# Kernel optimization log

Hardware: AMD Instinct MI355X
Metric: run time of the kernel (lower is better)

The kernel has to match this reference:

```python
import jax, jax.numpy as jnp
import numpy as np

HEAD_DIM = 128
INFTY_APPROX = 1e+30
ROTARY_BASE = 10000.0

B, T, M = 2, 2048, 1024
H = M // HEAD_DIM  # 8


def setup_inputs() -> dict:
    key = jax.random.key(0)
    ks = jax.random.split(key, 5)
    x = jax.random.normal(ks[0], (B, T, M), dtype=jnp.float32)
    # mu-param inits: wq zeros in the original; use small random here for a
    # non-degenerate numerical baseline, scaled like kv_init = d_model**-0.5
    scale = M ** (-0.5)
    wq = jax.random.normal(ks[1], (M, H, HEAD_DIM), dtype=jnp.float32) * scale
    wk = jax.random.normal(ks[2], (M, H, HEAD_DIM), dtype=jnp.float32) * scale
    wv = jax.random.normal(ks[3], (M, H, HEAD_DIM), dtype=jnp.float32) * scale
    wo = jax.random.normal(ks[4], (H, HEAD_DIM, M), dtype=jnp.float32) * scale
    return {"x": x, "wq": wq, "wk": wk, "wv": wv, "wo": wo}


def _rotary(x, base=ROTARY_BASE):
    # x: [..., T, W]; non-interpretable RoPE over even/odd halves of W
    length, width = x.shape[-2], x.shape[-1]
    half = width // 2
    positions = jnp.arange(length)[:, None].astype(x.dtype)          # [T,1]
    ang_freqs = jnp.power(base, -jnp.arange(half) / half)[None, :]   # [1,half]
    radians = positions * ang_freqs                                  # [T,half]
    cos = jnp.cos(radians).astype(x.dtype)
    sin = jnp.sin(radians).astype(x.dtype)
    even, odd = jnp.split(x, 2, axis=-1)
    return jnp.concatenate([even * cos - odd * sin,
                            even * sin + odd * cos], axis=-1)


def _fractional_rotary(x):
    # rotary on first half of head dim, passthrough on the rest
    rot, skip = jnp.split(x, 2, axis=-1)
    return jnp.concatenate([_rotary(rot), skip], axis=-1)


def reference(x, wq, wk, wv, wo):
    q = jnp.einsum('bim,mhd->bhid', x, wq)
    k = jnp.einsum('bim,mhd->bhid', x, wk)
    v = jnp.einsum('bim,mhd->bhid', x, wv)
    q = _fractional_rotary(q)
    k = _fractional_rotary(k)
    # mu-param attention: scale by 1/HEAD_DIM (not 1/sqrt(D))
    s = jnp.einsum('bhid,bhjd->bhij', q, k) / HEAD_DIM
    i = jnp.arange(T)[:, None]
    j = jnp.arange(T)[None, :]
    mask = (i < j).astype(s.dtype)  # strictly-upper-triangular
    s = s - jnp.asarray(INFTY_APPROX, dtype=s.dtype) * mask
    p = jax.nn.softmax(s, axis=-1)
    o = jnp.einsum('bhij,bhjd->bhid', p, v)
    r = jnp.einsum('bhid,hdm->bim', o, wo)
    return r
```

## Files before the change

kernel.cpp:

```cpp
#include <hip/hip_runtime.h>

#define T_SEQ 2048
#define MDL   1024
#define NH    8
#define HD    128

typedef __bf16 bf16;
typedef __bf16 bf16x8 __attribute__((ext_vector_type(8)));
typedef __bf16 bf16x4 __attribute__((ext_vector_type(4)));
typedef float  f32x4  __attribute__((ext_vector_type(4)));

#define GLB(p) ((const __attribute__((address_space(1))) void*)(p))
#define LDS(p) ((__attribute__((address_space(3))) void*)(p))


__global__ __launch_bounds__(256) void convert_x_kernel(
    const float* __restrict__ x, bf16* __restrict__ xb)
{
    size_t i = ((size_t)blockIdx.x * 256 + threadIdx.x) * 8;
    float4 v0 = *(const float4*)(x + i);
    float4 v1 = *(const float4*)(x + i + 4);
    bf16x8 o;
    o[0]=(bf16)v0.x; o[1]=(bf16)v0.y; o[2]=(bf16)v0.z; o[3]=(bf16)v0.w;
    o[4]=(bf16)v1.x; o[5]=(bf16)v1.y; o[6]=(bf16)v1.z; o[7]=(bf16)v1.w;
    *(bf16x8*)(xb + i) = o;
}

__global__ __launch_bounds__(256) void transpose_w_kernel(
    const float* __restrict__ wq, const float* __restrict__ wk,
    const float* __restrict__ wv, const float* __restrict__ wo,
    bf16* __restrict__ Wt, bf16* __restrict__ Wot)
{
    __shared__ bf16 t_lds[64 * 72];
    const int bx = blockIdx.x;
    const int sec = bx >> 8;
    const int tile = bx & 255;
    const int k0 = (tile >> 4) * 64, n0 = (tile & 15) * 64;
    const float* src = sec == 0 ? wq : sec == 1 ? wk : sec == 2 ? wv : wo;
    bf16* dst = sec < 3 ? (Wt + (size_t)sec * MDL * MDL) : Wot;

    const int tid = threadIdx.x;
    const int ir = tid >> 2, jc = (tid & 3) * 16;
    const float* sp = src + (size_t)(k0 + ir) * MDL + n0 + jc;
    #pragma unroll
    for (int c = 0; c < 4; ++c) {
        float4 v = *(const float4*)(sp + c * 4);
        bf16x4 o; o[0]=(bf16)v.x; o[1]=(bf16)v.y; o[2]=(bf16)v.z; o[3]=(bf16)v.w;
        *(bf16x4*)&t_lds[ir * 72 + jc + c * 4] = o;
    }
    __syncthreads();
    bf16x8 o0, o1;
    #pragma unroll
    for (int jj = 0; jj < 8; ++jj) {
        o0[jj] = t_lds[(jc + jj) * 72 + ir];
        o1[jj] = t_lds[(jc + 8 + jj) * 72 + ir];
    }
    bf16* dp = dst + (size_t)(n0 + ir) * MDL + k0 + jc;
    *(bf16x8*)dp = o0;
    *(bf16x8*)(dp + 8) = o1;
}

__global__ __launch_bounds__(256) void qkv_rope_kernel(
    const bf16* __restrict__ xb, const bf16* __restrict__ Wt,
    bf16* __restrict__ Qb, bf16* __restrict__ Kt, bf16* __restrict__ Vt)
{
    __shared__ bf16 smem[8192];
    bf16* a_lds = smem;
    bf16* b_lds = smem + 4096;

    const int tid = threadIdx.x, bx = blockIdx.x;
    const int nt = bx % 24, mt = bx / 24;
    const int n0 = nt * 128, m0 = mt * 128;
    const int section = n0 >> 10;
    const int h = (n0 & 1023) >> 7;

    const int lane = tid & 63, w = tid >> 6;
    const int quad = lane >> 4, l15 = lane & 15;
    const int wr = w >> 1, wc = w & 1;
    const int lrow = lane >> 2, lsub = lane & 3;

    const bf16* gA = xb + (size_t)m0 * MDL + lsub * 8;
    const bf16* gB = Wt + (size_t)n0 * MDL + lsub * 8;

    f32x4 acc[4][4] = {};

    for (int k0 = 0; k0 < MDL; k0 += 32) {
        #pragma unroll
        for (int i = 0; i < 2; ++i) {
            const int ch = w * 2 + i;
            const int row = ch * 16 + lrow;
            __builtin_amdgcn_global_load_lds(GLB(gA + (size_t)row * MDL + k0),
                                             LDS(&a_lds[ch * 16 * 32]), 16, 0, 0);
            __builtin_amdgcn_global_load_lds(GLB(gB + (size_t)row * MDL + k0),
                                             LDS(&b_lds[ch * 16 * 32]), 16, 0, 0);
        }
        __syncthreads();

        bf16x8 af[4], bfr[4];
        #pragma unroll
        for (int mi = 0; mi < 4; ++mi)
            af[mi] = *(const bf16x8*)&a_lds[(wr * 64 + mi * 16 + l15) * 32 + quad * 8];
        #pragma unroll
        for (int ni = 0; ni < 4; ++ni)
            bfr[ni] = *(const bf16x8*)&b_lds[(wc * 64 + ni * 16 + l15) * 32 + quad * 8];
        #pragma unroll
        for (int mi = 0; mi < 4; ++mi)
            #pragma unroll
            for (int ni = 0; ni < 4; ++ni)
                acc[mi][ni] = __builtin_amdgcn_mfma_f32_16x16x32_bf16(af[mi], bfr[ni], acc[mi][ni], 0, 0, 0);
        __syncthreads();
    }

    const int bdx = m0 >> 11;
    const int t0 = m0 & (T_SEQ - 1);
    const int bh = bdx * NH + h;

    if (section == 2) {
        #pragma unroll
        for (int c = 0; c < 2; ++c) {
            if (wc == c) {
                #pragma unroll
                for (int mi = 0; mi < 4; ++mi)
                    #pragma unroll
                    for (int r = 0; r < 4; ++r) {
                        int t_loc = wr * 64 + mi * 16 + quad * 4 + r;
                        int base = (t_loc >> 3) * 512 + (t_loc & 7);
                        #pragma unroll
                        for (int ni = 0; ni < 4; ++ni)
                            smem[base + (ni * 16 + l15) * 8] = (bf16)acc[mi][ni][r];
                    }
            }
            __syncthreads();
            {
                const int t8 = tid >> 4;
                bf16* vp = Vt + ((size_t)(bh * 32 + (t0 >> 6) + (t8 >> 3))) * 8192
                              + (t8 & 7) * 1024 + c * 512 + (tid & 15) * 32;
                #pragma unroll
                for (int k = 0; k < 4; ++k)
                    *(bf16x8*)(vp + k * 8) = *(const bf16x8*)&smem[tid * 32 + k * 8];
            }
            __syncthreads();
        }
        return;
    }

    float fr_n[2];
    #pragma unroll
    for (int ni = 0; ni < 2; ++ni)
        fr_n[ni] = __expf(-(float)(ni * 16 + l15) * 0.28782313662425573f);

    if (section == 0) {
        #pragma unroll
        for (int mi = 0; mi < 4; ++mi) {
            #pragma unroll
            for (int r = 0; r < 4; ++r) {
                int t = t0 + wr * 64 + mi * 16 + quad * 4 + r;
                bf16* orow = Qb + ((size_t)bh * T_SEQ + t) * HD;
                if (wc == 0) {
                    #pragma unroll
                    for (int ni = 0; ni < 2; ++ni) {
                        int d = ni * 16 + l15;
                        float ang = (float)t * fr_n[ni];
                        float sn = __sinf(ang), cs = __cosf(ang);
                        float ev = acc[mi][ni][r];
                        float ov = acc[mi][ni + 2][r];
                        orow[d]      = (bf16)(ev * cs - ov * sn);
                        orow[d + 32] = (bf16)(ev * sn + ov * cs);
                    }
                } else {
                    #pragma unroll
                    for (int ni = 0; ni < 4; ++ni)
                        orow[64 + ni * 16 + l15] = (bf16)acc[mi][ni][r];
                }
            }
        }
    } else {
        #pragma unroll
        for (int c = 0; c < 2; ++c) {
            if (wr == c) {
                #pragma unroll
                for (int mi = 0; mi < 4; ++mi) {
                    #pragma unroll
                    for (int r = 0; r < 4; ++r) {
                        int tl = mi * 16 + quad * 4 + r;
                        int t = t0 + c * 64 + tl;
                        if (wc == 0) {
                            #pragma unroll
                            for (int ni = 0; ni < 2; ++ni) {
                                int d = ni * 16 + l15;
                                float ang = (float)t * fr_n[ni];
                                float sn = __sinf(ang), cs = __cosf(ang);
                                float ev = acc[mi][ni][r];
                                float ov = acc[mi][ni + 2][r];
                                smem[(d >> 3) * 512 + tl * 8 + (d & 7)] = (bf16)(ev * cs - ov * sn);
                                int d2 = d + 32;
                                smem[(d2 >> 3) * 512 + tl * 8 + (d2 & 7)] = (bf16)(ev * sn + ov * cs);
                            }
                        } else {
                            #pragma unroll
                            for (int ni = 0; ni < 4; ++ni) {
                                int d = 64 + ni * 16 + l15;
                                smem[(d >> 3) * 512 + tl * 8 + (d & 7)] = (bf16)acc[mi][ni][r];
                            }
                        }
                    }
                }
            }
            __syncthreads();
            {
                bf16* kp = Kt + ((size_t)(bh * 32 + (t0 >> 6) + c)) * 8192 + tid * 32;
                #pragma unroll
                for (int k = 0; k < 4; ++k)
                    *(bf16x8*)(kp + k * 8) = *(const bf16x8*)&smem[tid * 32 + k * 8];
            }
            __syncthreads();
        }
    }
}

__global__ __launch_bounds__(256) void attn_kernel(
    const bf16* __restrict__ Qb, const bf16* __restrict__ Kt,
    const bf16* __restrict__ Vt, bf16* __restrict__ PO, float* __restrict__ Pl)
{
    __shared__ bf16 k_lds[8192];
    __shared__ bf16 v_lds[8192];
    __shared__ bf16 p_lds[4][32 * 72];

    const int tid = threadIdx.x, lane = tid & 63, w = tid >> 6;
    const int quad = lane >> 4, l15 = lane & 15;
    const int bx = blockIdx.x;
    const int s0 = bx & 3;
    const int ip = (bx >> 2) & 7;
    const int bh = bx >> 5;
    const int tA = 2 * ip + 2;

    const bf16* Kbh = Kt + (size_t)bh * 32 * 8192;
    const bf16* Vbh = Vt + (size_t)bh * 32 * 8192;

    bf16x8 qf[2][4];
    f32x4 Of[2][8];
    float l_r[2][4];

    int g = s0;

    #pragma unroll 1
    for (int phase = 0; phase < 2; ++phase) {
        const int qt = (phase == 0) ? ip : 15 - ip;
        const int gend = (phase == 0) ? tA : 34;
        const int gbase = (phase == 0) ? 0 : tA;
        if (g >= gend) continue;

        #pragma unroll
        for (int mi = 0; mi < 2; ++mi) {
            const bf16* qrow = Qb + ((size_t)bh * T_SEQ + qt * 128 + w * 32 + mi * 16 + l15) * HD + quad * 8;
            #pragma unroll
            for (int kk = 0; kk < 4; ++kk)
                qf[mi][kk] = *(const bf16x8*)(qrow + kk * 32);
            #pragma unroll
            for (int di = 0; di < 8; ++di) Of[mi][di] = (f32x4){0.f, 0.f, 0.f, 0.f};
            #pragma unroll
            for (int r = 0; r < 4; ++r) l_r[mi][r] = 0.f;
        }

        #pragma unroll 1
        for (; g < gend; g += 4) {
            const int jt = g - gbase;
            __syncthreads();
            const bf16* ktile = Kbh + jt * 8192;
            const bf16* vtile = Vbh + jt * 8192;
            #pragma unroll
            for (int ii = 0; ii < 4; ++ii) {
                const int j = w * 4 + ii;
                __builtin_amdgcn_global_load_lds(GLB(ktile + j * 512 + lane * 8),
                                                 LDS(&k_lds[j * 512]), 16, 0, 0);
                __builtin_amdgcn_global_load_lds(GLB(vtile + j * 512 + lane * 8),
                                                 LDS(&v_lds[j * 512]), 16, 0, 0);
            }
            __syncthreads();

            f32x4 sa[2][4] = {};
            #pragma unroll
            for (int kk = 0; kk < 4; ++kk) {
                bf16x8 kb[4];
                #pragma unroll
                for (int ni = 0; ni < 4; ++ni)
                    kb[ni] = *(const bf16x8*)&k_lds[(kk * 4 + quad) * 512 + (ni * 16 + l15) * 8];
                #pragma unroll
                for (int ni = 0; ni < 4; ++ni)
                    #pragma unroll
                    for (int mi = 0; mi < 2; ++mi)
                        sa[mi][ni] = __builtin_amdgcn_mfma_f32_16x16x32_bf16(qf[mi][kk], kb[ni], sa[mi][ni], 0, 0, 0);
            }

            const bool diag = (jt >= 2 * qt);
            #pragma unroll
            for (int mi = 0; mi < 2; ++mi) {
                const int rowb = w * 32 + mi * 16 + quad * 4;
                #pragma unroll
                for (int r = 0; r < 4; ++r) {
                    float ps = 0.f;
                    #pragma unroll
                    for (int ni = 0; ni < 4; ++ni) {
                        float pv = __expf(sa[mi][ni][r] * 0.0078125f);
                        if (diag && (jt * 64 + ni * 16 + l15) > (qt * 128 + rowb + r)) pv = 0.f;
                        ps += pv;
                        p_lds[w][(mi * 16 + quad * 4 + r) * 72 + ni * 16 + l15] = (bf16)pv;
                    }
                    l_r[mi][r] += ps;
                }
            }

            #pragma unroll
            for (int kk = 0; kk < 2; ++kk) {
                bf16x8 pa[2];
                #pragma unroll
                for (int mi = 0; mi < 2; ++mi)
                    pa[mi] = *(const bf16x8*)&p_lds[w][(mi * 16 + l15) * 72 + kk * 32 + quad * 8];
                #pragma unroll
                for (int di = 0; di < 8; ++di) {
                    bf16x8 vb = *(const bf16x8*)&v_lds[(kk * 4 + quad) * 1024 + (di * 16 + l15) * 8];
                    #pragma unroll
                    for (int mi = 0; mi < 2; ++mi)
                        Of[mi][di] = __builtin_amdgcn_mfma_f32_16x16x32_bf16(pa[mi], vb, Of[mi][di], 0, 0, 0);
                }
            }
        }

        const size_t slot = ((size_t)bh * 16 + qt) * 4 + s0;
        #pragma unroll
        for (int mi = 0; mi < 2; ++mi) {
            #pragma unroll
            for (int r = 0; r < 4; ++r) {
                float ls = l_r[mi][r];
                ls += __shfl_xor(ls, 1); ls += __shfl_xor(ls, 2);
                ls += __shfl_xor(ls, 4); ls += __shfl_xor(ls, 8);
                const int row = w * 32 + mi * 16 + quad * 4 + r;
                if (l15 == 0) Pl[slot * 128 + row] = ls;
                bf16* pr = PO + (slot * 128 + row) * 128;
                #pragma unroll
                for (int di = 0; di < 8; ++di)
                    pr[di * 16 + l15] = (bf16)Of[mi][di][r];
            }
        }
    }
}

__global__ __launch_bounds__(256) void attn_combine_kernel(
    const bf16* __restrict__ PO, const float* __restrict__ Pl,
    bf16* __restrict__ Ob)
{
    const int idx = blockIdx.x * 256 + threadIdx.x;
    const int dcol = (idx & 15) * 8;
    const int rowg = idx >> 4;
    const int bh = rowg >> 11, qrow = rowg & 2047;
    const int qt = qrow >> 7, row = qrow & 127;
    const int ns = (qt == 0) ? 2 : 4;

    float acc[8] = {};
    float l = 0.f;
    for (int s = 0; s < ns; ++s) {
        const size_t base = (((size_t)bh * 16 + qt) * 4 + s) * 128 + row;
        bf16x8 po = *(const bf16x8*)&PO[base * 128 + dcol];
        #pragma unroll
        for (int jj = 0; jj < 8; ++jj) acc[jj] += (float)po[jj];
        l += Pl[base];
    }
    const float inv = 1.f / l;
    const int b = bh >> 3, hh = bh & 7, t = qt * 128 + row;
    bf16x8 o;
    #pragma unroll
    for (int jj = 0; jj < 8; ++jj) o[jj] = (bf16)(acc[jj] * inv);
    *(bf16x8*)(Ob + ((size_t)(b * T_SEQ + t) * NH + hh) * HD + dcol) = o;
}

__global__ __launch_bounds__(256) void out_proj_kernel(
    const bf16* __restrict__ Ob, const bf16* __restrict__ Wot,
    float* __restrict__ out)
{
    __shared__ bf16 a_lds[128 * 32];
    __shared__ bf16 b_lds[128 * 32];

    const int tid = threadIdx.x, bx = blockIdx.x;
    const int nt = bx & 7, mt = bx >> 3;
    const int n0 = nt * 128, m0 = mt * 128;

    const int lane = tid & 63, w = tid >> 6;
    const int quad = lane >> 4, l15 = lane & 15;
    const int wr = w >> 1, wc = w & 1;
    const int lrow = lane >> 2, lsub = lane & 3;

    const bf16* gA = Ob  + (size_t)m0 * MDL + lsub * 8;
    const bf16* gB = Wot + (size_t)n0 * MDL + lsub * 8;

    f32x4 acc[4][4] = {};

    for (int k0 = 0; k0 < MDL; k0 += 32) {
        #pragma unroll
        for (int i = 0; i < 2; ++i) {
            const int ch = w * 2 + i;
            const int row = ch * 16 + lrow;
            __builtin_amdgcn_global_load_lds(GLB(gA + (size_t)row * MDL + k0),
                                             LDS(&a_lds[ch * 16 * 32]), 16, 0, 0);
            __builtin_amdgcn_global_load_lds(GLB(gB + (size_t)row * MDL + k0),
                                             LDS(&b_lds[ch * 16 * 32]), 16, 0, 0);
        }
        __syncthreads();

        bf16x8 af[4], bfr[4];
        #pragma unroll
        for (int mi = 0; mi < 4; ++mi)
            af[mi] = *(const bf16x8*)&a_lds[(wr * 64 + mi * 16 + l15) * 32 + quad * 8];
        #pragma unroll
        for (int ni = 0; ni < 4; ++ni)
            bfr[ni] = *(const bf16x8*)&b_lds[(wc * 64 + ni * 16 + l15) * 32 + quad * 8];
        #pragma unroll
        for (int mi = 0; mi < 4; ++mi)
            #pragma unroll
            for (int ni = 0; ni < 4; ++ni)
                acc[mi][ni] = __builtin_amdgcn_mfma_f32_16x16x32_bf16(af[mi], bfr[ni], acc[mi][ni], 0, 0, 0);
        __syncthreads();
    }

    #pragma unroll
    for (int mi = 0; mi < 4; ++mi)
        #pragma unroll
        for (int r = 0; r < 4; ++r) {
            int row_g = m0 + wr * 64 + mi * 16 + quad * 4 + r;
            float* crow = out + (size_t)row_g * MDL + n0;
            #pragma unroll
            for (int ni = 0; ni < 4; ++ni)
                crow[wc * 64 + ni * 16 + l15] = acc[mi][ni][r];
        }
}

extern "C" void kernel_launch(void* const* d_in, const int* in_sizes, int n_in,
                              void* d_out, int out_size, void* d_ws, size_t ws_size,
                              hipStream_t stream) {
    const float* x  = (const float*)d_in[0];
    const float* wq = (const float*)d_in[1];
    const float* wk = (const float*)d_in[2];
    const float* wv = (const float*)d_in[3];
    const float* wo = (const float*)d_in[4];
    float* out = (float*)d_out;

    const size_t NTOK = (size_t)2 * NH * T_SEQ * HD;
    bf16*  Qb  = (bf16*)d_ws;
    bf16*  Kt  = Qb + NTOK;
    bf16*  Vt  = Kt + NTOK;
    bf16*  Ob  = Vt + NTOK;
    bf16*  Wot = Ob + NTOK;
    bf16*  PO  = Wot + (size_t)MDL * MDL;
    float* Pl  = (float*)(PO + (size_t)16 * 16 * 4 * 128 * 128);

    bf16* xbuf = (bf16*)d_out;
    bf16* Wt   = xbuf + (size_t)4096 * MDL;

    transpose_w_kernel<<<1024, 256, 0, stream>>>(wq, wk, wv, wo, Wt, Wot);
    convert_x_kernel<<<2048, 256, 0, stream>>>(x, xbuf);
    qkv_rope_kernel<<<768, 256, 0, stream>>>(xbuf, Wt, Qb, Kt, Vt);
    attn_kernel<<<512, 256, 0, stream>>>(Qb, Kt, Vt, PO, Pl);
    attn_combine_kernel<<<2048, 256, 0, stream>>>(PO, Pl, Ob);
    out_proj_kernel<<<256, 256, 0, stream>>>(Ob, Wot, out);
}
```

Before: 207.5 us.

## Increase attention split-K to six, fold softmax scale into Q, vectorize P stores

Raises the number of KV splits per query-tile pair from 4 to 6, launching 768 attention blocks instead of 512 so more CUs are busy, and sizes the partial-output buffers and the combine kernel to match. Q is pre-multiplied by log2(e)/128 at projection time so the softmax can use a raw exp2 with no per-element multiply. V's LDS write layout is permuted so that P can be written to LDS as packed 4-wide bf16 vectors instead of scalar stores. The costs are a larger partial-output workspace and more combine traffic, and the V and P layout permutations must stay consistent with each other.

```diff
diff --git a/kernel.cpp b/kernel.cpp
--- a/kernel.cpp
+++ b/kernel.cpp
@@ -4,6 +4,7 @@
 #define MDL   1024
 #define NH    8
 #define HD    128
+#define SPLIT 6
 
 typedef __bf16 bf16;
 typedef __bf16 bf16x8 __attribute__((ext_vector_type(8)));
@@ -12,6 +13,14 @@
 
 #define GLB(p) ((const __attribute__((address_space(1))) void*)(p))
 #define LDS(p) ((__attribute__((address_space(3))) void*)(p))
+
+#if __has_builtin(__builtin_amdgcn_exp2f)
+#define EXP2(x) __builtin_amdgcn_exp2f(x)
+#else
+#define EXP2(x) __expf((x) * 0.6931471805599453f)
+#endif
+
+#define QSCALE 0.011271055f
 
 
 __global__ __launch_bounds__(256) void convert_x_kernel(
@@ -123,8 +132,8 @@
                 for (int mi = 0; mi < 4; ++mi)
                     #pragma unroll
                     for (int r = 0; r < 4; ++r) {
-                        int t_loc = wr * 64 + mi * 16 + quad * 4 + r;
-                        int base = (t_loc >> 3) * 512 + (t_loc & 7);
+                        int p = 16 * quad + 4 * r + mi;
+                        int base = (wr * 8 + (p >> 3)) * 512 + (p & 7);
                         #pragma unroll
                         for (int ni = 0; ni < 4; ++ni)
                             smem[base + (ni * 16 + l15) * 8] = (bf16)acc[mi][ni][r];
@@ -164,13 +173,13 @@
                         float sn = __sinf(ang), cs = __cosf(ang);
                         float ev = acc[mi][ni][r];
                         float ov = acc[mi][ni + 2][r];
-                        orow[d]      = (bf16)(ev * cs - ov * sn);
-                        orow[d + 32] = (bf16)(ev * sn + ov * cs);
+                        orow[d]      = (bf16)((ev * cs - ov * sn) * QSCALE);
+                        orow[d + 32] = (bf16)((ev * sn + ov * cs) * QSCALE);
                     }
                 } else {
                     #pragma unroll
                     for (int ni = 0; ni < 4; ++ni)
-                        orow[64 + ni * 16 + l15] = (bf16)acc[mi][ni][r];
+                        orow[64 + ni * 16 + l15] = (bf16)(acc[mi][ni][r] * QSCALE);
                 }
             }
         }
@@ -229,9 +238,9 @@
     const int tid = threadIdx.x, lane = tid & 63, w = tid >> 6;
     const int quad = lane >> 4, l15 = lane & 15;
     const int bx = blockIdx.x;
-    const int s0 = bx & 3;
-    const int ip = (bx >> 2) & 7;
-    const int bh = bx >> 5;
+    const int s0 = bx % SPLIT;
+    const int ip = (bx / SPLIT) & 7;
+    const int bh = bx / (SPLIT * 8);
     const int tA = 2 * ip + 2;
 
     const bf16* Kbh = Kt + (size_t)bh * 32 * 8192;
@@ -263,7 +272,7 @@
         }
 
         #pragma unroll 1
-        for (; g < gend; g += 4) {
+        for (; g < gend; g += SPLIT) {
             const int jt = g - gbase;
             __syncthreads();
             const bf16* ktile = Kbh + jt * 8192;
@@ -299,13 +308,15 @@
                 #pragma unroll
                 for (int r = 0; r < 4; ++r) {
                     float ps = 0.f;
+                    bf16x4 pq;
                     #pragma unroll
                     for (int ni = 0; ni < 4; ++ni) {
-                        float pv = __expf(sa[mi][ni][r] * 0.0078125f);
+                        float pv = EXP2(sa[mi][ni][r]);
                         if (diag && (jt * 64 + ni * 16 + l15) > (qt * 128 + rowb + r)) pv = 0.f;
                         ps += pv;
-                        p_lds[w][(mi * 16 + quad * 4 + r) * 72 + ni * 16 + l15] = (bf16)pv;
+                        pq[ni] = (bf16)pv;
                     }
+                    *(bf16x4*)&p_lds[w][(mi * 16 + quad * 4 + r) * 72 + l15 * 4] = pq;
                     l_r[mi][r] += ps;
                 }
             }
@@ -326,7 +337,7 @@
             }
         }
 
-        const size_t slot = ((size_t)bh * 16 + qt) * 4 + s0;
+        const size_t slot = ((size_t)bh * 16 + qt) * SPLIT + s0;
         #pragma unroll
         for (int mi = 0; mi < 2; ++mi) {
             #pragma unroll
@@ -354,12 +365,12 @@
     const int rowg = idx >> 4;
     const int bh = rowg >> 11, qrow = rowg & 2047;
     const int qt = qrow >> 7, row = qrow & 127;
-    const int ns = (qt == 0) ? 2 : 4;
+    const int ns = (qt == 0) ? 2 : ((qt == 1) ? 4 : SPLIT);
 
     float acc[8] = {};
     float l = 0.f;
     for (int s = 0; s < ns; ++s) {
-        const size_t base = (((size_t)bh * 16 + qt) * 4 + s) * 128 + row;
+        const size_t base = (((size_t)bh * 16 + qt) * SPLIT + s) * 128 + row;
         bf16x8 po = *(const bf16x8*)&PO[base * 128 + dcol];
         #pragma unroll
         for (int jj = 0; jj < 8; ++jj) acc[jj] += (float)po[jj];
@@ -450,7 +461,7 @@
     bf16*  Ob  = Vt + NTOK;
     bf16*  Wot = Ob + NTOK;
     bf16*  PO  = Wot + (size_t)MDL * MDL;
-    float* Pl  = (float*)(PO + (size_t)16 * 16 * 4 * 128 * 128);
+    float* Pl  = (float*)(PO + (size_t)16 * 16 * SPLIT * 128 * 128);
 
     bf16* xbuf = (bf16*)d_out;
     bf16* Wt   = xbuf + (size_t)4096 * MDL;
@@ -458,7 +469,7 @@
     transpose_w_kernel<<<1024, 256, 0, stream>>>(wq, wk, wv, wo, Wt, Wot);
     convert_x_kernel<<<2048, 256, 0, stream>>>(x, xbuf);
     qkv_rope_kernel<<<768, 256, 0, stream>>>(xbuf, Wt, Qb, Kt, Vt);
-    attn_kernel<<<512, 256, 0, stream>>>(Qb, Kt, Vt, PO, Pl);
+    attn_kernel<<<16 * 8 * SPLIT, 256, 0, stream>>>(Qb, Kt, Vt, PO, Pl);
     attn_combine_kernel<<<2048, 256, 0, stream>>>(PO, Pl, Ob);
     out_proj_kernel<<<256, 256, 0, stream>>>(Ob, Wot, out);
 }
```

New measurement: 207.9 us. Within noise of the previous version (+0.2%).
